# Kernel optimization log

Measured on AMD Instinct MI355X. Metric: run time of the kernel, lower is better.

Reference implementation:

```python
import jax, jax.numpy as jnp
import numpy as np

E, B, T = 8, 8, 1024
DIN = 640    # hidden_state_dim + conf_dim
DH = 1024    # 2 * hidden_state_dim
DOUT = 128   # 1024 // num_experts (slicing=True)
CODE = 256
TAU = 0.1
IMPORTANCE_REG = 0.01
EPS = 1e-8


def setup_inputs() -> dict:
    key = jax.random.key(0)
    ks = jax.random.split(key, 9)
    h = jax.random.normal(ks[0], (B, T, DIN), jnp.float32)
    code_emb = jax.random.normal(ks[1], (B, T, CODE), jnp.float32)
    u = jax.random.uniform(ks[2], (B, T, E), jnp.float32, 1e-6, 1.0 - 1e-6)
    gumbel_noise = -jnp.log(-jnp.log(u))
    code_anchor = jax.random.normal(ks[3], (E, CODE), jnp.float32)
    feature_importance = jax.random.normal(ks[4], (E, DIN), jnp.float32)
    W1 = jax.random.normal(ks[5], (E, DIN, DH), jnp.float32) * 0.02
    b1 = jax.random.normal(ks[6], (E, DH), jnp.float32) * 0.02
    W2 = jax.random.normal(ks[7], (E, DH, DOUT), jnp.float32) * 0.02
    b2 = jax.random.normal(ks[8], (E, DOUT), jnp.float32) * 0.02
    return {"h": h, "code_emb": code_emb, "gumbel_noise": gumbel_noise,
            "code_anchor": code_anchor, "feature_importance": feature_importance,
            "W1": W1, "b1": b1, "W2": W2, "b2": b2}


def _l2norm(x, axis):
    n = jnp.sqrt(jnp.sum(x * x, axis=axis, keepdims=True))
    return x / jnp.maximum(n, 1e-12)


def reference(h, code_emb, gumbel_noise, code_anchor, feature_importance, W1, b1, W2, b2):
    # router logits: cosine similarity between code_emb and code anchors  [B,T,E]
    anchor_n = _l2norm(code_anchor, axis=1)
    code_n = _l2norm(code_emb, axis=-1)
    router_logits = jnp.einsum('btd,ed->bte', code_n, anchor_n)
    # gumbel-softmax, tau=0.1, hard=False (noise provided for determinism)
    expert_weights = jax.nn.softmax((router_logits + gumbel_noise) / TAU, axis=-1)  # [B,T,E]
    # temperature-scaled importance softmax; importance_temperature=0.5, clamp no-op
    temp = jnp.clip(jnp.float32(0.5), 0.1, 5.0)
    importance = jax.nn.softmax(feature_importance / temp, axis=1)  # [E,DIN]
    # per-expert importance-weighted inputs [B,E,T,DIN]
    weighted_h = h[:, None, :, :] * importance[None, :, None, :]
    # all experts as one batched 2-layer MLP (exact GELU like torch nn.GELU)
    hid = jax.nn.gelu(jnp.einsum('betd,edh->beth', weighted_h, W1) + b1[None, :, None, :],
                      approximate=False)
    expert_outputs = jnp.einsum('beth,eho->beto', hid, W2) + b2[None, :, None, :]  # [B,E,T,DOUT]
    # slicing combine: expert i fills output slice [i*DOUT:(i+1)*DOUT], scaled by its gate
    gated = expert_outputs.transpose(0, 2, 1, 3) * expert_weights[..., None]  # [B,T,E,DOUT]
    full_output = gated.reshape(B, T, E * DOUT)  # [B,T,1024]
    # routing aux loss
    expert_counts = expert_weights.sum(0)  # [T,E]
    expert_load = expert_counts / (expert_counts.sum() + EPS)
    routing_loss = 0.5 * (jnp.std(expert_counts, ddof=1)
                          + (-expert_load * jnp.log(expert_load + EPS)).sum())
    imp_entropy = -(importance * jnp.log(importance + EPS)).sum(-1)  # [E]
    aux_loss = routing_loss + IMPORTANCE_REG * imp_entropy.mean()
    # diversity loss on raw feature_importance
    sim = feature_importance @ feature_importance.T  # [E,E]
    off = sim * (1.0 - jnp.eye(E, dtype=sim.dtype))
    diversity_loss = (off ** 2).sum() / (E * (E - 1))
    imp_mean = importance.mean(-1)
    imp_std = jnp.std(importance, axis=-1, ddof=1)
    return full_output, aux_loss, diversity_loss, imp_entropy, imp_mean, imp_std
```

## Files before the change

### kernel.cpp

```cpp
#include <hip/hip_runtime.h>
#include <math.h>

#define DIN 640
#define DH 1024
#define DOUT 128
#define CODEDIM 256
#define NE 8
#define NB 8
#define NT 1024
#define NTOK 8192
#define TAU_INV 10.0f
#define FEPS 1e-8f

#define AUX_OFF  8388608
#define DIV_OFF  8388609
#define ENT_OFF  8388610
#define MEAN_OFF 8388618
#define STD_OFF  8388626

typedef __bf16 bf16;
typedef bf16 bf16x8 __attribute__((ext_vector_type(8)));
typedef float f32x4 __attribute__((ext_vector_type(4)));

__device__ __forceinline__ float gelu(float x) {
  return 0.5f * x * (1.0f + erff(x * 0.70710678118654752f));
}

#define BAR() do { asm volatile("" ::: "memory"); __builtin_amdgcn_s_barrier(); asm volatile("" ::: "memory"); } while(0)
#define VMCNT6 asm volatile("s_waitcnt vmcnt(6)" ::: "memory")
#define VMCNT0 asm volatile("s_waitcnt vmcnt(0)" ::: "memory")

__device__ __forceinline__ void gload16(const void* g, void* l) {
  __builtin_amdgcn_global_load_lds(
      (const __attribute__((address_space(1))) unsigned int*)g,
      (__attribute__((address_space(3))) unsigned int*)l, 16, 0, 0);
}

__device__ __forceinline__ float blk_sum(float v, float* sb) {
  #pragma unroll
  for (int o = 32; o > 0; o >>= 1) v += __shfl_down(v, o, 64);
  __syncthreads();
  if ((threadIdx.x & 63) == 0) sb[threadIdx.x >> 6] = v;
  __syncthreads();
  float tot = 0.f;
  int nw = blockDim.x >> 6;
  for (int i = 0; i < nw; ++i) tot += sb[i];
  return tot;
}

__device__ __forceinline__ float blk_max(float v, float* sb) {
  #pragma unroll
  for (int o = 32; o > 0; o >>= 1) v = fmaxf(v, __shfl_down(v, o, 64));
  __syncthreads();
  if ((threadIdx.x & 63) == 0) sb[threadIdx.x >> 6] = v;
  __syncthreads();
  float m = -3.0e38f;
  int nw = blockDim.x >> 6;
  for (int i = 0; i < nw; ++i) m = fmaxf(m, sb[i]);
  return m;
}

__global__ __launch_bounds__(256)
void k_prep(const float* __restrict__ h, const float* __restrict__ ce,
            const float* __restrict__ gn, const float* __restrict__ ca,
            const float* __restrict__ fi, const float* __restrict__ W1,
            const float* __restrict__ W2,
            bf16* __restrict__ w1t, bf16* __restrict__ w2t,
            bf16* __restrict__ xb, float* __restrict__ ew,
            float* __restrict__ out) {
  const int bid = blockIdx.x;
  const int tid = threadIdx.x;
  if (bid < 1280) {
    __shared__ float tile[64][65];
    __shared__ float sb[8];
    __shared__ float red[2];
    int c0 = (bid & 15) * 64;
    int r0 = ((bid >> 4) % 10) * 64;
    int ee = bid / 160;
    const float* s = W1 + (size_t)ee*DIN*DH;
    bf16* d = w1t + (size_t)ee*DH*DIN;
    int i2v = tid + 512;
    float v0 = fi[ee*DIN + tid] * 2.0f;
    float v1 = fi[ee*DIN + tid + 256] * 2.0f;
    float v2 = (i2v < DIN) ? fi[ee*DIN + i2v] * 2.0f : -3.0e38f;
    float m = blk_max(fmaxf(v0, fmaxf(v1, v2)), sb);
    float se = expf(v0 - m) + expf(v1 - m) + ((i2v < DIN) ? expf(v2 - m) : 0.f);
    float ssum = blk_sum(se, sb);
    if (tid == 0) { red[0] = m; red[1] = 1.0f / ssum; }
    int tx = tid & 63, ty = tid >> 6;
    #pragma unroll
    for (int p = 0; p < 16; ++p) {
      int r = p*4 + ty;
      tile[r][tx] = s[(size_t)(r0 + r)*DH + c0 + tx];
    }
    __syncthreads();
    float sc = expf(fi[ee*DIN + r0 + tx]*2.0f - red[0]) * red[1];
    #pragma unroll
    for (int p = 0; p < 16; ++p) {
      int cr = p*4 + ty;
      d[(size_t)(c0 + cr)*DIN + r0 + tx] = (bf16)(tile[tx][cr] * sc);
    }
  } else if (bid < 1536) {
    __shared__ float tile[64][65];
    int c = bid - 1280;
    int c0 = (c & 1) * 64;
    int r0 = ((c >> 1) & 15) * 64;
    int ee = c >> 5;
    const float* s = W2 + (size_t)ee*DH*DOUT;
    bf16* d = w2t + (size_t)ee*DOUT*DH;
    int tx = tid & 63, ty = tid >> 6;
    #pragma unroll
    for (int p = 0; p < 16; ++p) {
      int r = p*4 + ty;
      tile[r][tx] = s[(size_t)(r0 + r)*DOUT + c0 + tx];
    }
    __syncthreads();
    #pragma unroll
    for (int p = 0; p < 16; ++p) {
      int cr = p*4 + ty;
      d[(size_t)(c0 + cr)*DH + r0 + tx] = (bf16)tile[tx][cr];
    }
  } else if (bid < 4096) {
    size_t i = (size_t)(bid - 1536)*256 + tid;
    const float4* p = (const float4*)(h + i*8);
    float4 u0 = p[0], u1 = p[1];
    bf16x8 o;
    o[0]=(bf16)u0.x; o[1]=(bf16)u0.y; o[2]=(bf16)u0.z; o[3]=(bf16)u0.w;
    o[4]=(bf16)u1.x; o[5]=(bf16)u1.y; o[6]=(bf16)u1.z; o[7]=(bf16)u1.w;
    *(bf16x8*)(xb + i*8) = o;
  } else if (bid < 6144) {
    __shared__ float anc[NE*CODEDIM];
    __shared__ float sd[256];
    __shared__ float invn[8];
    int c = bid - 4096;
    for (int i = tid; i < NE*CODEDIM; i += 256) anc[i] = ca[i];
    __syncthreads();
    {
      int e8 = tid >> 5, base = e8*CODEDIM + (tid & 31)*8;
      float ps = 0.f;
      #pragma unroll
      for (int j = 0; j < 8; ++j) { float v = anc[base + j]; ps += v*v; }
      sd[tid] = ps;
    }
    __syncthreads();
    if (tid < 8) {
      float s2 = 0.f;
      for (int j = 0; j < 32; ++j) s2 += sd[tid*32 + j];
      invn[tid] = 1.0f / fmaxf(sqrtf(s2), 1e-12f);
    }
    __syncthreads();
    int wv = tid >> 6, lane = tid & 63;
    int token = c*4 + wv;
    float4 x = *(const float4*)(ce + (size_t)token*CODEDIM + lane*4);
    float ss = x.x*x.x + x.y*x.y + x.z*x.z + x.w*x.w;
    #pragma unroll
    for (int o = 1; o < 64; o <<= 1) ss += __shfl_xor(ss, o, 64);
    float invx = 1.0f / fmaxf(sqrtf(ss), 1e-12f);
    const float* g = gn + (size_t)token*NE;
    float z[8];
    float m = -3.0e38f;
    #pragma unroll
    for (int e2 = 0; e2 < NE; ++e2) {
      const float* a = anc + e2*CODEDIM + lane*4;
      float d = x.x*a[0] + x.y*a[1] + x.z*a[2] + x.w*a[3];
      #pragma unroll
      for (int o = 1; o < 64; o <<= 1) d += __shfl_xor(d, o, 64);
      z[e2] = (d * invx * invn[e2] + g[e2]) * TAU_INV;
      m = fmaxf(m, z[e2]);
    }
    float ssum = 0.f;
    float pz[8];
    #pragma unroll
    for (int e2 = 0; e2 < NE; ++e2) { pz[e2] = expf(z[e2] - m); ssum += pz[e2]; }
    float num = 0.f;
    #pragma unroll
    for (int e2 = 0; e2 < NE; ++e2) num = (lane == e2) ? pz[e2] : num;
    if (lane < NE) ew[(size_t)token*NE + lane] = num / ssum;
  } else if (bid < 6152) {
    __shared__ float sb[8];
    int e = bid - 6144;
    int d2v = tid + 512;
    float v0 = fi[e*DIN + tid] * 2.0f;
    float v1 = fi[e*DIN + tid + 256] * 2.0f;
    float v2 = (d2v < DIN) ? fi[e*DIN + d2v] * 2.0f : -3.0e38f;
    float m = blk_max(fmaxf(v0, fmaxf(v1, v2)), sb);
    float e0 = expf(v0 - m), e1 = expf(v1 - m);
    float e2 = (d2v < DIN) ? expf(v2 - m) : 0.f;
    float s = blk_sum(e0 + e1 + e2, sb);
    float inv = 1.0f / s;
    float p0 = e0*inv, p1 = e1*inv, p2 = e2*inv;
    float ok2 = (d2v < DIN) ? 1.f : 0.f;
    float sp  = p0 + p1 + ok2*p2;
    float sp2 = p0*p0 + p1*p1 + ok2*p2*p2;
    float sent = p0*logf(p0 + FEPS) + p1*logf(p1 + FEPS) + ok2*p2*logf(p2 + FEPS);
    sp   = blk_sum(sp, sb);
    sp2  = blk_sum(sp2, sb);
    sent = blk_sum(sent, sb);
    if (tid == 0) {
      out[ENT_OFF + e]  = -sent;
      out[MEAN_OFF + e] = sp * (1.0f/DIN);
      float var = (sp2 - sp*sp*(1.0f/DIN)) * (1.0f/(DIN-1));
      out[STD_OFF + e]  = sqrtf(fmaxf(var, 0.f));
    }
  } else {
    __shared__ float sd[256];
    int p = tid >> 2, q = tid & 3;
    int i = p >> 3, j = p & 7;
    float dot = 0.f;
    for (int d = q*160; d < q*160 + 160; ++d) dot += fi[i*DIN + d] * fi[j*DIN + d];
    sd[tid] = dot;
    __syncthreads();
    if (tid < 64) {
      float s = sd[tid*4] + sd[tid*4+1] + sd[tid*4+2] + sd[tid*4+3];
      int ii = tid >> 3, jj = tid & 7;
      float val = (ii != jj) ? s*s : 0.f;
      #pragma unroll
      for (int o = 32; o > 0; o >>= 1) val += __shfl_down(val, o, 64);
      if (tid == 0) out[DIV_OFF] = val * (1.0f/56.0f);
    }
  }
}

#define G1_LDS 34816
__global__ __launch_bounds__(256, 3)
void k_g1(const bf16* __restrict__ xb, const bf16* __restrict__ w1t,
          const float* __restrict__ b1, bf16* __restrict__ Hb, int ebase) {
  __shared__ __align__(16) char L[G1_LDS];
  const int bid = blockIdx.x;
  const int el = bid & 3, e = ebase + el;
  const int nt = (bid >> 2) & 7, mt = bid >> 5;
  const int M0 = mt * 128, N0 = nt * 128;
  const int tid = threadIdx.x;
  const int lane = tid & 63, w = tid >> 6;
  const int l15 = lane & 15, g4 = lane >> 4;
  const int wr = w >> 1, wc = w & 1;

  const char* gAsrc[4];
  const char* gBsrc[4];
  #pragma unroll
  for (int j = 0; j < 4; ++j) {
    unsigned p = (unsigned)((w*4 + j)*1024 + lane*16);
    unsigned q = p ^ (((p >> 7) & 7u) << 4);
    gAsrc[j] = (const char*)xb + (size_t)(M0 + (int)(q >> 7))*(DIN*2) + (q & 127u);
    gBsrc[j] = (const char*)w1t + (size_t)(e*DH + N0 + (int)(q >> 7))*(DIN*2) + (q & 127u);
  }

  unsigned afOff[4][2], bfOff[4][2];
  #pragma unroll
  for (int mi = 0; mi < 4; ++mi)
    #pragma unroll
    for (int kk = 0; kk < 2; ++kk) {
      int row = wr*64 + mi*16 + l15;
      int slot = kk*4 + g4;
      afOff[mi][kk] = (unsigned)(row*128 + ((slot ^ (row & 7)) << 4));
    }
  #pragma unroll
  for (int ni = 0; ni < 4; ++ni)
    #pragma unroll
    for (int kk = 0; kk < 2; ++kk) {
      int row = wc*64 + ni*16 + l15;
      int slot = kk*4 + g4;
      bfOff[ni][kk] = (unsigned)(16384 + row*128 + ((slot ^ (row & 7)) << 4));
    }

  f32x4 acc[4][4] = {};
  for (int t = 0; t < 10; ++t) {
    if (t) BAR();
    size_t ko = (size_t)t * 128;
    #pragma unroll
    for (int j = 0; j < 4; ++j) {
      gload16(gAsrc[j] + ko, L + (w*4 + j)*1024);
      gload16(gBsrc[j] + ko, L + 16384 + (w*4 + j)*1024);
    }
    VMCNT0;
    BAR();
    #pragma unroll
    for (int kk = 0; kk < 2; ++kk) {
      bf16x8 af[4], bfr[4];
      #pragma unroll
      for (int mi = 0; mi < 4; ++mi) af[mi] = *(const bf16x8*)(L + afOff[mi][kk]);
      #pragma unroll
      for (int ni = 0; ni < 4; ++ni) bfr[ni] = *(const bf16x8*)(L + bfOff[ni][kk]);
      #pragma unroll
      for (int mi = 0; mi < 4; ++mi)
        #pragma unroll
        for (int ni = 0; ni < 4; ++ni)
          acc[mi][ni] = __builtin_amdgcn_mfma_f32_16x16x32_bf16(
              af[mi], bfr[ni], acc[mi][ni], 0, 0, 0);
    }
  }
  BAR();
  float b1v[4];
  #pragma unroll
  for (int ni = 0; ni < 4; ++ni)
    b1v[ni] = b1[e*DH + N0 + wc*64 + ni*16 + l15];
  #pragma unroll
  for (int mi = 0; mi < 4; ++mi)
    #pragma unroll
    for (int ni = 0; ni < 4; ++ni)
      #pragma unroll
      for (int r = 0; r < 4; ++r) {
        float v = gelu(acc[mi][ni][r] + b1v[ni]);
        int row = wr*64 + mi*16 + g4*4 + r;
        int col = wc*64 + ni*16 + l15;
        *(bf16*)(L + row*272 + col*2) = (bf16)v;
      }
  __syncthreads();
  #pragma unroll
  for (int j = 0; j < 8; ++j) {
    int c = j*256 + tid;
    int row = c >> 4, slot = c & 15;
    bf16x8 v = *(const bf16x8*)(L + row*272 + slot*16);
    *(bf16x8*)((char*)Hb + (size_t)(el*NTOK + M0 + row)*(DH*2) + (size_t)N0*2 + slot*16) = v;
  }
}

__global__ __launch_bounds__(256, 3)
void k_g2(const bf16* __restrict__ Hb, const bf16* __restrict__ w2t,
          const float* __restrict__ b2, const float* __restrict__ ew,
          float* __restrict__ out, int ebase) {
  __shared__ __align__(16) char L[49152];
  const int bid = blockIdx.x;
  const int el = bid & 3, e = ebase + el;
  const int mt = bid >> 2;
  const int M0 = mt * 64;
  const int tid = threadIdx.x;
  const int lane = tid & 63, w = tid >> 6;
  const int l15 = lane & 15, g4 = lane >> 4;
  const int nb = w * 32;

  const char* gAsrc[2];
  #pragma unroll
  for (int j = 0; j < 2; ++j) {
    unsigned p = (unsigned)((w*2 + j)*1024 + lane*16);
    unsigned q = p ^ (((p >> 7) & 7u) << 4);
    gAsrc[j] = (const char*)Hb + (size_t)(el*NTOK + M0 + (int)(q >> 7))*(DH*2) + (q & 127u);
  }
  const char* gBsrc[4];
  #pragma unroll
  for (int j = 0; j < 4; ++j) {
    unsigned p = (unsigned)((w*4 + j)*1024 + lane*16);
    unsigned q = p ^ (((p >> 7) & 7u) << 4);
    gBsrc[j] = (const char*)w2t + (size_t)(e*DOUT + (int)(q >> 7))*(DH*2) + (q & 127u);
  }
  auto STAGE = [&](int buf, int t) {
    size_t ko = (size_t)t * 128;
    #pragma unroll
    for (int j = 0; j < 2; ++j)
      gload16(gAsrc[j] + ko, L + buf*8192 + (w*2 + j)*1024);
    #pragma unroll
    for (int j = 0; j < 4; ++j)
      gload16(gBsrc[j] + ko, L + 16384 + buf*16384 + (w*4 + j)*1024);
  };

  unsigned afOff[4][2], bfOff[2][2];
  #pragma unroll
  for (int mi = 0; mi < 4; ++mi)
    #pragma unroll
    for (int kk = 0; kk < 2; ++kk) {
      int row = mi*16 + l15;
      int slot = kk*4 + g4;
      afOff[mi][kk] = (unsigned)(row*128 + ((slot ^ (row & 7)) << 4));
    }
  #pragma unroll
  for (int ni = 0; ni < 2; ++ni)
    #pragma unroll
    for (int kk = 0; kk < 2; ++kk) {
      int row = nb + ni*16 + l15;
      int slot = kk*4 + g4;
      bfOff[ni][kk] = (unsigned)(row*128 + ((slot ^ (row & 7)) << 4));
    }

  f32x4 acc[4][2] = {};
  STAGE(0, 0);
  for (int t = 0; t < 16; ++t) {
    int buf = t & 1;
    if (t < 15) { STAGE(buf ^ 1, t + 1); VMCNT6; } else { VMCNT0; }
    BAR();
    const char* Ab = L + buf*8192;
    const char* Bb = L + 16384 + buf*16384;
    #pragma unroll
    for (int kk = 0; kk < 2; ++kk) {
      bf16x8 af[4], bfr[2];
      #pragma unroll
      for (int mi = 0; mi < 4; ++mi) af[mi] = *(const bf16x8*)(Ab + afOff[mi][kk]);
      #pragma unroll
      for (int ni = 0; ni < 2; ++ni) bfr[ni] = *(const bf16x8*)(Bb + bfOff[ni][kk]);
      #pragma unroll
      for (int mi = 0; mi < 4; ++mi)
        #pragma unroll
        for (int ni = 0; ni < 2; ++ni)
          acc[mi][ni] = __builtin_amdgcn_mfma_f32_16x16x32_bf16(
              af[mi], bfr[ni], acc[mi][ni], 0, 0, 0);
    }
    BAR();
  }
  float b2v[2];
  #pragma unroll
  for (int ni = 0; ni < 2; ++ni)
    b2v[ni] = b2[e*DOUT + nb + ni*16 + l15];
  float gt[4][4];
  #pragma unroll
  for (int mi = 0; mi < 4; ++mi)
    #pragma unroll
    for (int r = 0; r < 4; ++r)
      gt[mi][r] = ew[(size_t)(M0 + mi*16 + g4*4 + r)*NE + e];
  #pragma unroll
  for (int mi = 0; mi < 4; ++mi)
    #pragma unroll
    for (int ni = 0; ni < 2; ++ni)
      #pragma unroll
      for (int r = 0; r < 4; ++r) {
        int tok = M0 + mi*16 + g4*4 + r;
        int o = nb + ni*16 + l15;
        out[(size_t)tok*(NE*DOUT) + e*DOUT + o] = (acc[mi][ni][r] + b2v[ni]) * gt[mi][r];
      }
}

__global__ void k_counts(const float* __restrict__ ew, float* __restrict__ counts,
                         float* __restrict__ partials) {
  __shared__ float sb[4];
  int g2 = blockIdx.x*256 + threadIdx.x;
  float c = 0.f;
  #pragma unroll
  for (int b = 0; b < NB; ++b) c += ew[b*(NT*NE) + g2];
  counts[g2] = c;
  float tot = blk_sum(c, sb);
  if (threadIdx.x == 0) partials[blockIdx.x] = tot;
}

__global__ void k_aux(const float* __restrict__ counts, const float* __restrict__ partials,
                      float* __restrict__ out) {
  __shared__ float sb[4];
  int tid = threadIdx.x;
  float pv = (tid < 32) ? partials[tid] : 0.f;
  float total = blk_sum(pv, sb);
  float invt = 1.0f / (total + FEPS);
  float sq = 0.f, ent = 0.f;
  for (int i2 = tid; i2 < NT*NE; i2 += 256) {
    float c = counts[i2];
    sq += c*c;
    float ld = c * invt;
    ent -= ld * logf(ld + FEPS);
  }
  sq = blk_sum(sq, sb);
  ent = blk_sum(ent, sb);
  if (tid == 0) {
    float var = (sq - total*total*(1.0f/(NT*NE))) * (1.0f/(NT*NE - 1));
    float stdv = sqrtf(fmaxf(var, 0.f));
    float ment = 0.f;
    #pragma unroll
    for (int e2 = 0; e2 < NE; ++e2) ment += out[ENT_OFF + e2];
    ment *= (1.0f/NE);
    out[AUX_OFF] = 0.5f*(stdv + ent) + 0.01f*ment;
  }
}

extern "C" void kernel_launch(void* const* d_in, const int* in_sizes, int n_in,
                              void* d_out, int out_size, void* d_ws, size_t ws_size,
                              hipStream_t stream) {
  const float* h  = (const float*)d_in[0];
  const float* ce = (const float*)d_in[1];
  const float* gn = (const float*)d_in[2];
  const float* ca = (const float*)d_in[3];
  const float* fi = (const float*)d_in[4];
  const float* W1 = (const float*)d_in[5];
  const float* b1 = (const float*)d_in[6];
  const float* W2 = (const float*)d_in[7];
  const float* b2 = (const float*)d_in[8];
  float* out = (float*)d_out;
  char* ws = (char*)d_ws;
  bf16*  w1t      = (bf16*)(ws);
  bf16*  w2t      = (bf16*)(ws + 10485760);
  bf16*  xbuf     = (bf16*)(ws + 12582912);
  float* ew       = (float*)(ws + 23097344);
  float* counts   = (float*)(ws + 23359488);
  float* partials = (float*)(ws + 23392256);
  bf16*  Hbuf     = (bf16*)(ws + 23396352);

  k_prep<<<dim3(6153), dim3(256), 0, stream>>>(h, ce, gn, ca, fi, W1, W2,
                                               w1t, w2t, xbuf, ew, out);
  k_g1<<<dim3(2048), dim3(256), 0, stream>>>(xbuf, w1t, b1, Hbuf, 0);
  k_g2<<<dim3(512), dim3(256), 0, stream>>>(Hbuf, w2t, b2, ew, out, 0);
  k_g1<<<dim3(2048), dim3(256), 0, stream>>>(xbuf, w1t, b1, Hbuf, 4);
  k_g2<<<dim3(512), dim3(256), 0, stream>>>(Hbuf, w2t, b2, ew, out, 4);
  k_counts<<<dim3(32), dim3(256), 0, stream>>>(ew, counts, partials);
  k_aux<<<dim3(1), dim3(256), 0, stream>>>(counts, partials, out);
}
```

Before: 187.6 us.

## Enlarge first GEMM tile to 256x256 with double-buffered LDS prefetch

The first-layer expert GEMM moves from 128x128 tiles with 256 threads to 256x256 tiles with 512 threads (8 waves). LDS is now double-buffered so the next K-slice loads while the current one feeds MFMA, and s_setprio raises priority around the MFMA bursts. This aims to hide global-load latency and raise data reuse per loaded byte. In exchange each block uses about 130KB of LDS, so only one block fits per CU, the grid shrinks to 512 blocks, and register pressure from 32 accumulators per wave goes up.

```diff
diff --git a/kernel.cpp b/kernel.cpp
--- a/kernel.cpp
+++ b/kernel.cpp
@@ -221,96 +221,122 @@
   }
 }
 
-#define G1_LDS 34816
-__global__ __launch_bounds__(256, 3)
+#define G1_LDS 133120
+__global__ __launch_bounds__(512, 2)
 void k_g1(const bf16* __restrict__ xb, const bf16* __restrict__ w1t,
           const float* __restrict__ b1, bf16* __restrict__ Hb, int ebase) {
   __shared__ __align__(16) char L[G1_LDS];
   const int bid = blockIdx.x;
   const int el = bid & 3, e = ebase + el;
-  const int nt = (bid >> 2) & 7, mt = bid >> 5;
-  const int M0 = mt * 128, N0 = nt * 128;
+  const int nt = (bid >> 2) & 3, mt = bid >> 4;
+  const int M0 = mt * 256, N0 = nt * 256;
   const int tid = threadIdx.x;
   const int lane = tid & 63, w = tid >> 6;
   const int l15 = lane & 15, g4 = lane >> 4;
-  const int wr = w >> 1, wc = w & 1;
-
-  const char* gAsrc[4];
-  const char* gBsrc[4];
-  #pragma unroll
-  for (int j = 0; j < 4; ++j) {
-    unsigned p = (unsigned)((w*4 + j)*1024 + lane*16);
+  const int wr = w >> 2, wc = w & 3;
+
+  int rq[2], cq[2];
+  #pragma unroll
+  for (int j = 0; j < 2; ++j) {
+    unsigned p = (unsigned)((w*2 + j)*1024 + lane*16);
     unsigned q = p ^ (((p >> 7) & 7u) << 4);
-    gAsrc[j] = (const char*)xb + (size_t)(M0 + (int)(q >> 7))*(DIN*2) + (q & 127u);
-    gBsrc[j] = (const char*)w1t + (size_t)(e*DH + N0 + (int)(q >> 7))*(DIN*2) + (q & 127u);
-  }
-
-  unsigned afOff[4][2], bfOff[4][2];
-  #pragma unroll
-  for (int mi = 0; mi < 4; ++mi)
-    #pragma unroll
-    for (int kk = 0; kk < 2; ++kk) {
-      int row = wr*64 + mi*16 + l15;
-      int slot = kk*4 + g4;
-      afOff[mi][kk] = (unsigned)(row*128 + ((slot ^ (row & 7)) << 4));
-    }
-  #pragma unroll
-  for (int ni = 0; ni < 4; ++ni)
-    #pragma unroll
-    for (int kk = 0; kk < 2; ++kk) {
-      int row = wc*64 + ni*16 + l15;
-      int slot = kk*4 + g4;
-      bfOff[ni][kk] = (unsigned)(16384 + row*128 + ((slot ^ (row & 7)) << 4));
-    }
-
-  f32x4 acc[4][4] = {};
+    rq[j] = (int)(q >> 7);
+    cq[j] = (int)(q & 127u);
+  }
+  const char* gA[2];
+  const char* gB[2];
+  #pragma unroll
+  for (int j = 0; j < 2; ++j) {
+    gA[j] = (const char*)xb + (size_t)(M0 + rq[j])*(DIN*2) + cq[j];
+    gB[j] = (const char*)w1t + (size_t)(e*DH + N0 + rq[j])*(DIN*2) + cq[j];
+  }
+  auto STAGE_HALF = [&](int bb, int t, int hp) {
+    size_t ko = (size_t)t * 128;
+    if (hp < 2) {
+      size_t ro = (size_t)hp * 128 * (DIN*2);
+      char* dst = L + bb*32768 + hp*16384 + (w*2)*1024;
+      gload16(gA[0] + ro + ko, dst);
+      gload16(gA[1] + ro + ko, dst + 1024);
+    } else {
+      size_t ro = (size_t)(hp - 2) * 128 * (DIN*2);
+      char* dst = L + 65536 + bb*32768 + (hp - 2)*16384 + (w*2)*1024;
+      gload16(gB[0] + ro + ko, dst);
+      gload16(gB[1] + ro + ko, dst + 1024);
+    }
+  };
+
+  const unsigned s0 = (unsigned)((g4 ^ (l15 & 7)) << 4);
+  const unsigned s1 = (unsigned)(((4 + g4) ^ (l15 & 7)) << 4);
+  const unsigned aRow = (unsigned)((wr*128 + l15) * 128);
+  const unsigned bRow = (unsigned)((wc*64 + l15) * 128);
+
+  f32x4 acc[8][4] = {};
+
+  #pragma unroll
+  for (int hp = 0; hp < 4; ++hp) STAGE_HALF(0, 0, hp);
+  VMCNT0;
+  BAR();
+
   for (int t = 0; t < 10; ++t) {
-    if (t) BAR();
-    size_t ko = (size_t)t * 128;
-    #pragma unroll
-    for (int j = 0; j < 4; ++j) {
-      gload16(gAsrc[j] + ko, L + (w*4 + j)*1024);
-      gload16(gBsrc[j] + ko, L + 16384 + (w*4 + j)*1024);
+    const int cur = t & 1;
+    const unsigned aBase = (unsigned)(cur*32768) + aRow;
+    const unsigned bBase = (unsigned)(65536 + cur*32768) + bRow;
+    bf16x8 bfr[4][2];
+    #pragma unroll
+    for (int p = 0; p < 4; ++p) {
+      if (t < 9) STAGE_HALF(cur ^ 1, t + 1, p);
+      if (p == 0) {
+        #pragma unroll
+        for (int ni = 0; ni < 4; ++ni) {
+          bfr[ni][0] = *(const bf16x8*)(L + bBase + ni*2048 + s0);
+          bfr[ni][1] = *(const bf16x8*)(L + bBase + ni*2048 + s1);
+        }
+      }
+      bf16x8 af[2][2];
+      #pragma unroll
+      for (int m2 = 0; m2 < 2; ++m2) {
+        int mi = p*2 + m2;
+        af[m2][0] = *(const bf16x8*)(L + aBase + mi*2048 + s0);
+        af[m2][1] = *(const bf16x8*)(L + aBase + mi*2048 + s1);
+      }
+      __builtin_amdgcn_s_setprio(1);
+      #pragma unroll
+      for (int m2 = 0; m2 < 2; ++m2) {
+        int mi = p*2 + m2;
+        #pragma unroll
+        for (int ni = 0; ni < 4; ++ni) {
+          acc[mi][ni] = __builtin_amdgcn_mfma_f32_16x16x32_bf16(
+              af[m2][0], bfr[ni][0], acc[mi][ni], 0, 0, 0);
+          acc[mi][ni] = __builtin_amdgcn_mfma_f32_16x16x32_bf16(
+              af[m2][1], bfr[ni][1], acc[mi][ni], 0, 0, 0);
+        }
+      }
+      __builtin_amdgcn_s_setprio(0);
     }
     VMCNT0;
     BAR();
-    #pragma unroll
-    for (int kk = 0; kk < 2; ++kk) {
-      bf16x8 af[4], bfr[4];
-      #pragma unroll
-      for (int mi = 0; mi < 4; ++mi) af[mi] = *(const bf16x8*)(L + afOff[mi][kk]);
-      #pragma unroll
-      for (int ni = 0; ni < 4; ++ni) bfr[ni] = *(const bf16x8*)(L + bfOff[ni][kk]);
-      #pragma unroll
-      for (int mi = 0; mi < 4; ++mi)
-        #pragma unroll
-        for (int ni = 0; ni < 4; ++ni)
-          acc[mi][ni] = __builtin_amdgcn_mfma_f32_16x16x32_bf16(
-              af[mi], bfr[ni], acc[mi][ni], 0, 0, 0);
-    }
-  }
-  BAR();
+  }
   float b1v[4];
   #pragma unroll
   for (int ni = 0; ni < 4; ++ni)
     b1v[ni] = b1[e*DH + N0 + wc*64 + ni*16 + l15];
   #pragma unroll
-  for (int mi = 0; mi < 4; ++mi)
+  for (int mi = 0; mi < 8; ++mi)
     #pragma unroll
     for (int ni = 0; ni < 4; ++ni)
       #pragma unroll
       for (int r = 0; r < 4; ++r) {
         float v = gelu(acc[mi][ni][r] + b1v[ni]);
-        int row = wr*64 + mi*16 + g4*4 + r;
+        int row = wr*128 + mi*16 + g4*4 + r;
         int col = wc*64 + ni*16 + l15;
-        *(bf16*)(L + row*272 + col*2) = (bf16)v;
+        *(bf16*)(L + row*520 + col*2) = (bf16)v;
       }
   __syncthreads();
   #pragma unroll
-  for (int j = 0; j < 8; ++j) {
-    int c = j*256 + tid;
-    int row = c >> 4, slot = c & 15;
-    bf16x8 v = *(const bf16x8*)(L + row*272 + slot*16);
+  for (int j = 0; j < 16; ++j) {
+    int c = j*512 + tid;
+    int row = c >> 5, slot = c & 31;
+    bf16x8 v = *(const bf16x8*)(L + row*520 + slot*16);
     *(bf16x8*)((char*)Hb + (size_t)(el*NTOK + M0 + row)*(DH*2) + (size_t)N0*2 + slot*16) = v;
   }
 }
@@ -480,9 +506,9 @@
 
   k_prep<<<dim3(6153), dim3(256), 0, stream>>>(h, ce, gn, ca, fi, W1, W2,
                                                w1t, w2t, xbuf, ew, out);
-  k_g1<<<dim3(2048), dim3(256), 0, stream>>>(xbuf, w1t, b1, Hbuf, 0);
+  k_g1<<<dim3(512), dim3(512), 0, stream>>>(xbuf, w1t, b1, Hbuf, 0);
   k_g2<<<dim3(512), dim3(256), 0, stream>>>(Hbuf, w2t, b2, ew, out, 0);
-  k_g1<<<dim3(2048), dim3(256), 0, stream>>>(xbuf, w1t, b1, Hbuf, 4);
+  k_g1<<<dim3(512), dim3(512), 0, stream>>>(xbuf, w1t, b1, Hbuf, 4);
   k_g2<<<dim3(512), dim3(256), 0, stream>>>(Hbuf, w2t, b2, ew, out, 4);
   k_counts<<<dim3(32), dim3(256), 0, stream>>>(ew, counts, partials);
   k_aux<<<dim3(1), dim3(256), 0, stream>>>(counts, partials, out);
```

Result: slower. 204.4 us (+9.0%).
